# Kernel optimization log

Measured on AMD Instinct MI355X. Metric: run time of the kernel, lower is better.

Reference implementation:

```python
import jax, jax.numpy as jnp
import numpy as np

NU, NI, E = 100000, 100000, 500000  # users, items, edges per edge type
DIN, DH, DOUT = 128, 256, 128


def setup_inputs() -> dict:
    key = jax.random.key(0)
    ks = jax.random.split(key, 18)
    f = lambda k, s: jax.random.normal(k, s, dtype=jnp.float32) * 0.02
    inp = {
        # node embedding tables (x_dict defaults to embedding weights)
        'emb_user': f(ks[0], (NU, DIN)),
        'emb_item': f(ks[1], (NI, DIN)),
        # conv1 params: relation user->item (dst=item) and item->user (dst=user)
        'W1_self_ui': f(ks[2], (DIN, DH)), 'W1_neigh_ui': f(ks[3], (DIN, DH)), 'b1_ui': jnp.zeros((DH,), jnp.float32),
        'W1_self_iu': f(ks[4], (DIN, DH)), 'W1_neigh_iu': f(ks[5], (DIN, DH)), 'b1_iu': jnp.zeros((DH,), jnp.float32),
        # conv2 params
        'W2_self_ui': f(ks[6], (DH, DOUT)), 'W2_neigh_ui': f(ks[7], (DH, DOUT)), 'b2_ui': jnp.zeros((DOUT,), jnp.float32),
        'W2_self_iu': f(ks[8], (DH, DOUT)), 'W2_neigh_iu': f(ks[9], (DH, DOUT)), 'b2_iu': jnp.zeros((DOUT,), jnp.float32),
        # edge lists: e1 = user->item edges, e2 = item->user edges
        'e1_src': jax.random.randint(ks[10], (E,), 0, NU),
        'e1_dst': jax.random.randint(ks[11], (E,), 0, NI),
        'e2_src': jax.random.randint(ks[12], (E,), 0, NI),
        'e2_dst': jax.random.randint(ks[13], (E,), 0, NU),
    }
    return inp


def _sage(h_src, h_dst, e_src, e_dst, W_self, W_neigh, b, n_dst):
    # DGL SAGEConv('mean'): fc_self(h_dst) + fc_neigh(mean_neighbors(h_src)) + bias
    msg = h_src[e_src]                                   # [E, d] gather
    ssum = jax.ops.segment_sum(msg, e_dst, num_segments=n_dst)          # [n_dst, d]
    deg = jax.ops.segment_sum(jnp.ones((e_src.shape[0], 1), h_src.dtype), e_dst, num_segments=n_dst)
    mean = ssum / jnp.maximum(deg, 1.0)                  # zero in-degree -> 0
    return h_dst @ W_self + mean @ W_neigh + b


def reference(emb_user, emb_item,
              W1_self_ui, W1_neigh_ui, b1_ui, W1_self_iu, W1_neigh_iu, b1_iu,
              W2_self_ui, W2_neigh_ui, b2_ui, W2_self_iu, W2_neigh_iu, b2_iu,
              e1_src, e1_dst, e2_src, e2_dst):
    # layer 1 (HeteroGraphConv: each ntype receives from exactly one relation)
    h1_item = jax.nn.leaky_relu(_sage(emb_user, emb_item, e1_src, e1_dst, W1_self_ui, W1_neigh_ui, b1_ui, NI))
    h1_user = jax.nn.leaky_relu(_sage(emb_item, emb_user, e2_src, e2_dst, W1_self_iu, W1_neigh_iu, b1_iu, NU))
    # layer 2
    h2_item = _sage(h1_user, h1_item, e1_src, e1_dst, W2_self_ui, W2_neigh_ui, b2_ui, NI)
    h2_user = _sage(h1_item, h1_user, e2_src, e2_dst, W2_self_iu, W2_neigh_iu, b2_iu, NU)
    return (h2_user, h2_item)
```

## Files before the change

kernel.cpp:

```cpp
#include <hip/hip_runtime.h>
#include <stdint.h>

typedef unsigned short u16;
typedef unsigned int   u32;
typedef __attribute__((ext_vector_type(8))) short bf16x8;
typedef __attribute__((ext_vector_type(4))) float f32x4;
typedef __attribute__((ext_vector_type(8))) unsigned short u16x8;

constexpr int NUc = 100000;
constexpr int NIc = 100000;
constexpr int Ec  = 500000;
constexpr int Mrows = 100000;
constexpr int NB  = (100000 + 255) / 256;

__device__ __forceinline__ u16 f2bf(float f) {
  u32 u = __float_as_uint(f);
  u += 0x7fffu + ((u >> 16) & 1u);
  return (u16)(u >> 16);
}
__device__ __forceinline__ float bf2f(u16 h) { return __uint_as_float(((u32)h) << 16); }

__global__ void prep_all(const float* __restrict__ eu, const float* __restrict__ ei,
                         const float* __restrict__ W1s_ui, const float* __restrict__ W1n_ui,
                         const float* __restrict__ W1s_iu, const float* __restrict__ W1n_iu,
                         const float* __restrict__ W2s_ui, const float* __restrict__ W2n_ui,
                         const float* __restrict__ W2s_iu, const float* __restrict__ W2n_iu,
                         u16* __restrict__ ue, u16* __restrict__ ie,
                         u16* __restrict__ Wt1_ui, u16* __restrict__ Wt1_iu,
                         u16* __restrict__ Wt2c_u, u16* __restrict__ Wt2c_i) {
  constexpr int N4 = NUc * 128 / 4;
  constexpr int TOT = 2 * N4 + 262144;
  int i = blockIdx.x * blockDim.x + threadIdx.x;
  const int stride = gridDim.x * blockDim.x;
  for (int t = i; t < TOT; t += stride) {
    if (t < 2 * N4) {
      const float* src = (t < N4) ? eu : ei;
      u16* dst = (t < N4) ? ue : ie;
      int c = (t < N4) ? t : t - N4;
      float4 v = reinterpret_cast<const float4*>(src)[c];
      ushort4 o;
      o.x = f2bf(v.x); o.y = f2bf(v.y); o.z = f2bf(v.z); o.w = f2bf(v.w);
      reinterpret_cast<ushort4*>(dst)[c] = o;
    } else {
      int j = t - 2 * N4;
      if (j < 131072) {
        const float* Ws = (j < 65536) ? W1s_ui : W1s_iu;
        const float* Wn = (j < 65536) ? W1n_ui : W1n_iu;
        u16* dst = (j < 65536) ? Wt1_ui : Wt1_iu;
        int q = j & 65535;
        int n = q >> 8, k = q & 255;
        dst[q] = f2bf(k < 128 ? Ws[k * 256 + n] : Wn[(k - 128) * 256 + n]);
      } else {
        int q = j - 131072;
        int which = q >> 16;
        int s = q & 65535;
        int c = s >> 8, k = s & 255;
        float v;
        if (which == 0) v = (c < 128) ? W2n_ui[k * 128 + c] : W2s_iu[k * 128 + (c - 128)];
        else            v = (c < 128) ? W2n_iu[k * 128 + c] : W2s_ui[k * 128 + (c - 128)];
        u16* dst = which ? Wt2c_i : Wt2c_u;
        dst[s] = f2bf(v);
      }
    }
  }
}

__global__ void hist_kernel(const int* __restrict__ e1_dst, const int* __restrict__ e2_dst,
                            int* __restrict__ ideg1, int* __restrict__ ideg2,
                            int* __restrict__ rank1, int* __restrict__ rank2) {
  int i = blockIdx.x * blockDim.x + threadIdx.x;
  const int stride = gridDim.x * blockDim.x;
  for (; i < 2 * Ec; i += stride) {
    if (i < Ec) rank1[i] = atomicAdd(&ideg1[e1_dst[i]], 1);
    else        rank2[i - Ec] = atomicAdd(&ideg2[e2_dst[i - Ec]], 1);
  }
}

__global__ void block_reduce2(const int* __restrict__ ideg1, const int* __restrict__ ideg2,
                              int* __restrict__ bsum1, int* __restrict__ bsum2, int n) {
  const int* deg = blockIdx.y ? ideg2 : ideg1;
  int* bsum = blockIdx.y ? bsum2 : bsum1;
  __shared__ int s[256];
  int t = threadIdx.x, i = blockIdx.x * 256 + t;
  s[t] = (i < n) ? deg[i] : 0;
  __syncthreads();
  for (int st = 128; st > 0; st >>= 1) { if (t < st) s[t] += s[t + st]; __syncthreads(); }
  if (t == 0) bsum[blockIdx.x] = s[0];
}

__global__ void scan_bsums2(const int* __restrict__ bsum1, const int* __restrict__ bsum2,
                            int* __restrict__ bscan1, int* __restrict__ bscan2, int nb) {
  const int* bsum = blockIdx.x ? bsum2 : bsum1;
  int* bscan = blockIdx.x ? bscan2 : bscan1;
  __shared__ int s[512];
  int t = threadIdx.x;
  int v0 = (t < nb) ? bsum[t] : 0;
  s[t] = v0;
  __syncthreads();
  for (int d = 1; d < 512; d <<= 1) {
    int v = (t >= d) ? s[t - d] : 0;
    __syncthreads();
    s[t] += v;
    __syncthreads();
  }
  if (t < nb) bscan[t] = s[t] - v0;
}

__global__ void scan_blocks2(const int* __restrict__ ideg1, const int* __restrict__ ideg2,
                             const int* __restrict__ bscan1, const int* __restrict__ bscan2,
                             int* __restrict__ off1, int* __restrict__ off2, int n) {
  const int* deg = blockIdx.y ? ideg2 : ideg1;
  const int* bscan = blockIdx.y ? bscan2 : bscan1;
  int* off = blockIdx.y ? off2 : off1;
  __shared__ int s[256];
  int t = threadIdx.x, i = blockIdx.x * 256 + t;
  int d = (i < n) ? deg[i] : 0;
  s[t] = d;
  __syncthreads();
  for (int st = 1; st < 256; st <<= 1) {
    int v = (t >= st) ? s[t - st] : 0;
    __syncthreads();
    s[t] += v;
    __syncthreads();
  }
  if (i < n) off[i] = bscan[blockIdx.x] + s[t] - d;
  if (i == 0) off[n] = Ec;
}

__global__ void fill_csr_kernel(const int* __restrict__ e1_src, const int* __restrict__ e1_dst,
                                const int* __restrict__ e2_src, const int* __restrict__ e2_dst,
                                const int* __restrict__ rank1, const int* __restrict__ rank2,
                                const int* __restrict__ off1, const int* __restrict__ off2,
                                int* __restrict__ csr1, int* __restrict__ csr2) {
  int i = blockIdx.x * blockDim.x + threadIdx.x;
  const int stride = gridDim.x * blockDim.x;
  for (; i < 2 * Ec; i += stride) {
    if (i < Ec) {
      int d = e1_dst[i];
      csr1[off1[d] + rank1[i]] = e1_src[i];
    } else {
      int e = i - Ec;
      int d = e2_dst[e];
      csr2[off2[d] + rank2[e]] = e2_src[e];
    }
  }
}

__global__ __launch_bounds__(256) void gather2(const u16* __restrict__ fA, const int* __restrict__ offA,
                                               const int* __restrict__ csrA, u16* __restrict__ outA,
                                               const u16* __restrict__ fB, const int* __restrict__ offB,
                                               const int* __restrict__ csrB, u16* __restrict__ outB) {
  const int wid  = (blockIdx.x * blockDim.x + threadIdx.x) >> 6;
  const int lane = threadIdx.x & 63;
  const u16* f; const int* off; const int* csr; u16* out; int r;
  if (wid < 100000)      { f = fA; off = offA; csr = csrA; out = outA; r = wid; }
  else if (wid < 200000) { f = fB; off = offB; csr = csrB; out = outB; r = wid - 100000; }
  else return;
  const int j0 = off[r], j1 = off[r + 1];
  const int colb = lane << 1;
  float ax = 0.f, ay = 0.f;
  for (int jb = j0; jb < j1; jb += 64) {
    int cnt = min(64, j1 - jb);
    int idx = (jb + lane < j1) ? csr[jb + lane] : 0;
    int t = 0;
    for (; t + 2 <= cnt; t += 2) {
      int s0 = __shfl(idx, t), s1 = __shfl(idx, t + 1);
      u32 v0 = *reinterpret_cast<const u32*>(f + (size_t)s0 * 128 + colb);
      u32 v1 = *reinterpret_cast<const u32*>(f + (size_t)s1 * 128 + colb);
      ax += __uint_as_float(v0 << 16);
      ay += __uint_as_float(v0 & 0xffff0000u);
      ax += __uint_as_float(v1 << 16);
      ay += __uint_as_float(v1 & 0xffff0000u);
    }
    if (t < cnt) {
      int s0 = __shfl(idx, t);
      u32 v0 = *reinterpret_cast<const u32*>(f + (size_t)s0 * 128 + colb);
      ax += __uint_as_float(v0 << 16);
      ay += __uint_as_float(v0 & 0xffff0000u);
    }
  }
  float rs = 1.0f / fmaxf((float)(j1 - j0), 1.0f);
  u32 o = (u32)f2bf(ax * rs) | ((u32)f2bf(ay * rs) << 16);
  *reinterpret_cast<u32*>(out + (size_t)r * 128 + colb) = o;
}

__global__ __launch_bounds__(256) void gather_final(
    const u16* __restrict__ pA, const int* __restrict__ offA, const int* __restrict__ csrA,
    const u16* __restrict__ sA, float* __restrict__ oA,
    const u16* __restrict__ pB, const int* __restrict__ offB, const int* __restrict__ csrB,
    const u16* __restrict__ sB, float* __restrict__ oB) {
  const int wid  = (blockIdx.x * blockDim.x + threadIdx.x) >> 6;
  const int lane = threadIdx.x & 63;
  const u16* f; const int* off; const int* csr; const u16* sf; float* out; int r;
  if (wid < 100000)      { f = pA; off = offA; csr = csrA; sf = sA; out = oA; r = wid; }
  else if (wid < 200000) { f = pB; off = offB; csr = csrB; sf = sB; out = oB; r = wid - 100000; }
  else return;
  const int j0 = off[r], j1 = off[r + 1];
  const int colb = lane << 1;
  float ax = 0.f, ay = 0.f;
  for (int jb = j0; jb < j1; jb += 64) {
    int cnt = min(64, j1 - jb);
    int idx = (jb + lane < j1) ? csr[jb + lane] : 0;
    int t = 0;
    for (; t + 2 <= cnt; t += 2) {
      int s0 = __shfl(idx, t), s1 = __shfl(idx, t + 1);
      u32 v0 = *reinterpret_cast<const u32*>(f + (size_t)s0 * 128 + colb);
      u32 v1 = *reinterpret_cast<const u32*>(f + (size_t)s1 * 128 + colb);
      ax += __uint_as_float(v0 << 16);
      ay += __uint_as_float(v0 & 0xffff0000u);
      ax += __uint_as_float(v1 << 16);
      ay += __uint_as_float(v1 & 0xffff0000u);
    }
    if (t < cnt) {
      int s0 = __shfl(idx, t);
      u32 v0 = *reinterpret_cast<const u32*>(f + (size_t)s0 * 128 + colb);
      ax += __uint_as_float(v0 << 16);
      ay += __uint_as_float(v0 & 0xffff0000u);
    }
  }
  float rs = 1.0f / fmaxf((float)(j1 - j0), 1.0f);
  u32 sv = *reinterpret_cast<const u32*>(sf + (size_t)r * 128 + colb);
  float2 o;
  o.x = ax * rs + __uint_as_float(sv << 16);
  o.y = ay * rs + __uint_as_float(sv & 0xffff0000u);
  *reinterpret_cast<float2*>(out + (size_t)r * 128 + colb) = o;
}

__device__ __forceinline__ void glds16(const void* g, void* l) {
  __builtin_amdgcn_global_load_lds((const __attribute__((address_space(1))) void*)g,
                                   (__attribute__((address_space(3))) void*)l, 16, 0, 0);
}

template<int NTAB, int EPI, int AST>
__global__ __launch_bounds__(256) void mfma_gemm2(
    const u16* __restrict__ A0a, const u16* __restrict__ A1a, const u16* __restrict__ Bta,
    const float* __restrict__ biasa, u16* __restrict__ out0a, u16* __restrict__ out1a,
    const u16* __restrict__ A0b, const u16* __restrict__ A1b, const u16* __restrict__ Btb,
    const float* __restrict__ biasb, u16* __restrict__ out0b, u16* __restrict__ out1b,
    int M)
{
  constexpr int K = 256, BK = 32, BM = 128;
  __shared__ __align__(16) u16 smem[8192];
  u16* As = smem;
  u16* Bs = smem + 4096;

  const bool zb = (blockIdx.z != 0);
  const u16* A0 = zb ? A0b : A0a;
  const u16* A1 = zb ? A1b : A1a;
  const u16* Bt = zb ? Btb : Bta;
  const float* bias = zb ? biasb : biasa;

  const int tid  = threadIdx.x;
  const int lane = tid & 63;
  const int w    = tid >> 6;
  const int wr   = w >> 1, wc = w & 1;
  const int gr0  = blockIdx.x * BM;
  const int gc0  = blockIdx.y * BM;

  f32x4 acc[4][4];
  #pragma unroll
  for (int m = 0; m < 4; ++m)
    #pragma unroll
    for (int n = 0; n < 4; ++n) acc[m][n] = (f32x4){0.f, 0.f, 0.f, 0.f};

  const int srow  = lane >> 2;
  const int sslot = lane & 3;

  for (int kt = 0; kt < K; kt += BK) {
    const u16* At = (NTAB == 2 && kt >= 128) ? A1 : A0;
    const int kbase = (NTAB == 2) ? (kt & 127) : kt;
    #pragma unroll
    for (int c = 0; c < 2; ++c) {
      int rl = w * 32 + c * 16 + srow;
      int swz = (sslot ^ ((rl >> 1) & 3)) << 3;
      int grow = gr0 + rl; grow = grow < M ? grow : M - 1;
      glds16(At + (size_t)grow * AST + kbase + swz, As + (size_t)(w * 32 + c * 16) * BK);
      glds16(Bt + (size_t)(gc0 + rl) * K + kt + swz, Bs + (size_t)(w * 32 + c * 16) * BK);
    }
    __syncthreads();

    bf16x8 af[4], bfr[4];
    #pragma unroll
    for (int m = 0; m < 4; ++m) {
      int row = wr * 64 + m * 16 + (lane & 15);
      int idx = (row << 5) + ((((lane >> 4) ^ ((row >> 1) & 3))) << 3);
      af[m] = *reinterpret_cast<const bf16x8*>(As + idx);
    }
    #pragma unroll
    for (int n = 0; n < 4; ++n) {
      int row = wc * 64 + n * 16 + (lane & 15);
      int idx = (row << 5) + ((((lane >> 4) ^ ((row >> 1) & 3))) << 3);
      bfr[n] = *reinterpret_cast<const bf16x8*>(Bs + idx);
    }
    #pragma unroll
    for (int m = 0; m < 4; ++m)
      #pragma unroll
      for (int n = 0; n < 4; ++n)
        acc[m][n] = __builtin_amdgcn_mfma_f32_16x16x32_bf16(af[m], bfr[n], acc[m][n], 0, 0, 0);
    __syncthreads();
  }

  u16* outp;
  if (EPI == 0) outp = zb ? out0b : out0a;
  else          outp = (blockIdx.y == 0) ? (zb ? out0b : out0a) : (zb ? out1b : out1a);
  const bool useBias = (EPI == 0) || (blockIdx.y == 1);

  const int cLane = lane & 15;
  const int rGrp  = (lane >> 4) << 2;
  for (int s = 0; s < 2; ++s) {
    if (wr == s) {
      #pragma unroll
      for (int n = 0; n < 4; ++n) {
        int lc = wc * 64 + n * 16 + cLane;
        float b = 0.f;
        if (useBias) b = (EPI == 0) ? bias[gc0 + lc] : bias[lc];
        #pragma unroll
        for (int m = 0; m < 4; ++m) {
          int lr = m * 16 + rGrp;
          #pragma unroll
          for (int r = 0; r < 4; ++r) {
            float v = acc[m][n][r] + b;
            if (EPI == 0) v = (v >= 0.f) ? v : 0.01f * v;
            smem[(lr + r) * 128 + lc] = f2bf(v);
          }
        }
      }
    }
    __syncthreads();
    #pragma unroll
    for (int pass = 0; pass < 4; ++pass) {
      int chunk = pass * 256 + tid;
      int row = chunk >> 4, c8 = chunk & 15;
      int G = gr0 + s * 64 + row;
      if (G < M) {
        u16x8 v = *reinterpret_cast<const u16x8*>(smem + row * 128 + c8 * 8);
        if (EPI == 0)
          *reinterpret_cast<u16x8*>(outp + (size_t)G * 256 + gc0 + c8 * 8) = v;
        else
          *reinterpret_cast<u16x8*>(outp + (size_t)G * 128 + c8 * 8) = v;
      }
    }
    if (s == 0) __syncthreads();
  }
}

extern "C" void kernel_launch(void* const* d_in, const int* in_sizes, int n_in,
                              void* d_out, int out_size, void* d_ws, size_t ws_size,
                              hipStream_t stream) {
  const float* emb_user    = (const float*)d_in[0];
  const float* emb_item    = (const float*)d_in[1];
  const float* W1_self_ui  = (const float*)d_in[2];
  const float* W1_neigh_ui = (const float*)d_in[3];
  const float* b1_ui       = (const float*)d_in[4];
  const float* W1_self_iu  = (const float*)d_in[5];
  const float* W1_neigh_iu = (const float*)d_in[6];
  const float* b1_iu       = (const float*)d_in[7];
  const float* W2_self_ui  = (const float*)d_in[8];
  const float* W2_neigh_ui = (const float*)d_in[9];
  const float* b2_ui       = (const float*)d_in[10];
  const float* W2_self_iu  = (const float*)d_in[11];
  const float* W2_neigh_iu = (const float*)d_in[12];
  const float* b2_iu       = (const float*)d_in[13];
  const int* e1_src = (const int*)d_in[14];
  const int* e1_dst = (const int*)d_in[15];
  const int* e2_src = (const int*)d_in[16];
  const int* e2_dst = (const int*)d_in[17];

  u16* p16 = (u16*)d_ws;
  u16* ue     = p16; p16 += (size_t)NUc * 128;
  u16* ie     = p16; p16 += (size_t)NIc * 128;
  u16* h1i    = p16; p16 += (size_t)NIc * 256;
  u16* h1u    = p16; p16 += (size_t)NUc * 256;
  u16* aggb_i = p16; p16 += (size_t)NIc * 128;
  u16* aggb_u = p16; p16 += (size_t)NUc * 128;
  u16* proj_i2u = p16; p16 += (size_t)NIc * 128;
  u16* self_i   = p16; p16 += (size_t)NIc * 128;
  u16* Wt1_ui  = p16; p16 += 256 * 256;
  u16* Wt1_iu  = p16; p16 += 256 * 256;
  u16* Wt2c_u  = p16; p16 += 256 * 256;
  u16* Wt2c_i  = p16; p16 += 256 * 256;
  u16* proj_u2i = aggb_i;
  u16* self_u   = aggb_u;
  int* ip    = (int*)p16;
  int* ideg1 = ip;  ip += NIc;
  int* ideg2 = ip;  ip += NUc;
  int* off1  = ip;  ip += NIc + 1;
  int* off2  = ip;  ip += NUc + 1;
  int* rank1 = ip;  ip += Ec;
  int* rank2 = ip;  ip += Ec;
  int* csr1  = ip;  ip += Ec;
  int* csr2  = ip;  ip += Ec;
  int* bsum1 = ip;  ip += 512;
  int* bscan1= ip;  ip += 512;
  int* bsum2 = ip;  ip += 512;
  int* bscan2= ip;  ip += 512;

  float* h2_user = (float*)d_out;
  float* h2_item = h2_user + (size_t)NUc * 128;

  dim3 blk(256);
  const int gather2Blocks = (200000 + 3) / 4;
  dim3 gemmGrid(782, 2, 2);

  hipMemsetAsync(ideg1, 0, sizeof(int) * (size_t)(NIc + NUc), stream);
  prep_all<<<4096, blk, 0, stream>>>(emb_user, emb_item,
                                     W1_self_ui, W1_neigh_ui, W1_self_iu, W1_neigh_iu,
                                     W2_self_ui, W2_neigh_ui, W2_self_iu, W2_neigh_iu,
                                     ue, ie, Wt1_ui, Wt1_iu, Wt2c_u, Wt2c_i);
  hist_kernel<<<1024, blk, 0, stream>>>(e1_dst, e2_dst, ideg1, ideg2, rank1, rank2);
  block_reduce2<<<dim3(NB, 2), blk, 0, stream>>>(ideg1, ideg2, bsum1, bsum2, NIc);
  scan_bsums2<<<2, 512, 0, stream>>>(bsum1, bsum2, bscan1, bscan2, NB);
  scan_blocks2<<<dim3(NB, 2), blk, 0, stream>>>(ideg1, ideg2, bscan1, bscan2, off1, off2, NIc);
  fill_csr_kernel<<<1024, blk, 0, stream>>>(e1_src, e1_dst, e2_src, e2_dst,
                                            rank1, rank2, off1, off2, csr1, csr2);

  gather2<<<gather2Blocks, blk, 0, stream>>>(ue, off1, csr1, aggb_i,
                                             ie, off2, csr2, aggb_u);
  mfma_gemm2<2, 0, 128><<<gemmGrid, blk, 0, stream>>>(
      ie, aggb_i, Wt1_ui, b1_ui, h1i, nullptr,
      ue, aggb_u, Wt1_iu, b1_iu, h1u, nullptr, Mrows);

  mfma_gemm2<1, 1, 256><<<gemmGrid, blk, 0, stream>>>(
      h1u, nullptr, Wt2c_u, b2_iu, proj_u2i, self_u,
      h1i, nullptr, Wt2c_i, b2_ui, proj_i2u, self_i, Mrows);

  gather_final<<<gather2Blocks, blk, 0, stream>>>(
      proj_u2i, off1, csr1, self_i, h2_item,
      proj_i2u, off2, csr2, self_u, h2_user);
}
```

Baseline: 390.3 us.

## Fuse prep and histogram kernels, unroll gathers by four, add nontemporal memory ops

Merges the bf16 conversion/weight-transpose kernel and the degree histogram kernel into one launch, with block ranges partitioned so the two run concurrently. Unrolls the CSR gather loops in both gather kernels to four outstanding row loads per iteration to raise memory-level parallelism. Adds nontemporal loads and stores for streaming data (embedding reads, edge arrays in CSR fill, final outputs, self-projection GEMM outputs) to reduce cache pollution. The nontemporal hints may hurt if the data is reused soon after, such as the self projections read back by gather_final.

```diff
diff --git a/kernel.cpp b/kernel.cpp
--- a/kernel.cpp
+++ b/kernel.cpp
@@ -5,6 +5,7 @@
 typedef unsigned int   u32;
 typedef __attribute__((ext_vector_type(8))) short bf16x8;
 typedef __attribute__((ext_vector_type(4))) float f32x4;
+typedef __attribute__((ext_vector_type(2))) float f32x2;
 typedef __attribute__((ext_vector_type(8))) unsigned short u16x8;
 
 constexpr int NUc = 100000;
@@ -20,59 +21,62 @@
 }
 __device__ __forceinline__ float bf2f(u16 h) { return __uint_as_float(((u32)h) << 16); }
 
-__global__ void prep_all(const float* __restrict__ eu, const float* __restrict__ ei,
-                         const float* __restrict__ W1s_ui, const float* __restrict__ W1n_ui,
-                         const float* __restrict__ W1s_iu, const float* __restrict__ W1n_iu,
-                         const float* __restrict__ W2s_ui, const float* __restrict__ W2n_ui,
-                         const float* __restrict__ W2s_iu, const float* __restrict__ W2n_iu,
-                         u16* __restrict__ ue, u16* __restrict__ ie,
-                         u16* __restrict__ Wt1_ui, u16* __restrict__ Wt1_iu,
-                         u16* __restrict__ Wt2c_u, u16* __restrict__ Wt2c_i) {
-  constexpr int N4 = NUc * 128 / 4;
-  constexpr int TOT = 2 * N4 + 262144;
-  int i = blockIdx.x * blockDim.x + threadIdx.x;
-  const int stride = gridDim.x * blockDim.x;
-  for (int t = i; t < TOT; t += stride) {
-    if (t < 2 * N4) {
-      const float* src = (t < N4) ? eu : ei;
-      u16* dst = (t < N4) ? ue : ie;
-      int c = (t < N4) ? t : t - N4;
-      float4 v = reinterpret_cast<const float4*>(src)[c];
-      ushort4 o;
-      o.x = f2bf(v.x); o.y = f2bf(v.y); o.z = f2bf(v.z); o.w = f2bf(v.w);
-      reinterpret_cast<ushort4*>(dst)[c] = o;
-    } else {
-      int j = t - 2 * N4;
-      if (j < 131072) {
-        const float* Ws = (j < 65536) ? W1s_ui : W1s_iu;
-        const float* Wn = (j < 65536) ? W1n_ui : W1n_iu;
-        u16* dst = (j < 65536) ? Wt1_ui : Wt1_iu;
-        int q = j & 65535;
-        int n = q >> 8, k = q & 255;
-        dst[q] = f2bf(k < 128 ? Ws[k * 256 + n] : Wn[(k - 128) * 256 + n]);
+constexpr int PREP_B = 4096;
+constexpr int HIST_B = 1024;
+__global__ void prep_hist(const float* __restrict__ eu, const float* __restrict__ ei,
+                          const float* __restrict__ W1s_ui, const float* __restrict__ W1n_ui,
+                          const float* __restrict__ W1s_iu, const float* __restrict__ W1n_iu,
+                          const float* __restrict__ W2s_ui, const float* __restrict__ W2n_ui,
+                          const float* __restrict__ W2s_iu, const float* __restrict__ W2n_iu,
+                          u16* __restrict__ ue, u16* __restrict__ ie,
+                          u16* __restrict__ Wt1_ui, u16* __restrict__ Wt1_iu,
+                          u16* __restrict__ Wt2c_u, u16* __restrict__ Wt2c_i,
+                          const int* __restrict__ e1_dst, const int* __restrict__ e2_dst,
+                          int* __restrict__ ideg1, int* __restrict__ ideg2,
+                          int* __restrict__ rank1, int* __restrict__ rank2) {
+  if (blockIdx.x < PREP_B) {
+    constexpr int N4 = NUc * 128 / 4;
+    constexpr int TOT = 2 * N4 + 262144;
+    int i = blockIdx.x * blockDim.x + threadIdx.x;
+    const int stride = PREP_B * 256;
+    for (int t = i; t < TOT; t += stride) {
+      if (t < 2 * N4) {
+        const float* src = (t < N4) ? eu : ei;
+        u16* dst = (t < N4) ? ue : ie;
+        int c = (t < N4) ? t : t - N4;
+        f32x4 v = __builtin_nontemporal_load(reinterpret_cast<const f32x4*>(src) + c);
+        ushort4 o;
+        o.x = f2bf(v.x); o.y = f2bf(v.y); o.z = f2bf(v.z); o.w = f2bf(v.w);
+        reinterpret_cast<ushort4*>(dst)[c] = o;
       } else {
-        int q = j - 131072;
-        int which = q >> 16;
-        int s = q & 65535;
-        int c = s >> 8, k = s & 255;
-        float v;
-        if (which == 0) v = (c < 128) ? W2n_ui[k * 128 + c] : W2s_iu[k * 128 + (c - 128)];
-        else            v = (c < 128) ? W2n_iu[k * 128 + c] : W2s_ui[k * 128 + (c - 128)];
-        u16* dst = which ? Wt2c_i : Wt2c_u;
-        dst[s] = f2bf(v);
+        int j = t - 2 * N4;
+        if (j < 131072) {
+          const float* Ws = (j < 65536) ? W1s_ui : W1s_iu;
+          const float* Wn = (j < 65536) ? W1n_ui : W1n_iu;
+          u16* dst = (j < 65536) ? Wt1_ui : Wt1_iu;
+          int q = j & 65535;
+          int n = q >> 8, k = q & 255;
+          dst[q] = f2bf(k < 128 ? Ws[k * 256 + n] : Wn[(k - 128) * 256 + n]);
+        } else {
+          int q = j - 131072;
+          int which = q >> 16;
+          int s = q & 65535;
+          int c = s >> 8, k = s & 255;
+          float v;
+          if (which == 0) v = (c < 128) ? W2n_ui[k * 128 + c] : W2s_iu[k * 128 + (c - 128)];
+          else            v = (c < 128) ? W2n_iu[k * 128 + c] : W2s_ui[k * 128 + (c - 128)];
+          u16* dst = which ? Wt2c_i : Wt2c_u;
+          dst[s] = f2bf(v);
+        }
       }
     }
-  }
-}
-
-__global__ void hist_kernel(const int* __restrict__ e1_dst, const int* __restrict__ e2_dst,
-                            int* __restrict__ ideg1, int* __restrict__ ideg2,
-                            int* __restrict__ rank1, int* __restrict__ rank2) {
-  int i = blockIdx.x * blockDim.x + threadIdx.x;
-  const int stride = gridDim.x * blockDim.x;
-  for (; i < 2 * Ec; i += stride) {
-    if (i < Ec) rank1[i] = atomicAdd(&ideg1[e1_dst[i]], 1);
-    else        rank2[i - Ec] = atomicAdd(&ideg2[e2_dst[i - Ec]], 1);
+  } else {
+    int i = (blockIdx.x - PREP_B) * blockDim.x + threadIdx.x;
+    const int stride = HIST_B * 256;
+    for (; i < 2 * Ec; i += stride) {
+      if (i < Ec) rank1[i] = atomicAdd(&ideg1[e1_dst[i]], 1);
+      else        rank2[i - Ec] = atomicAdd(&ideg2[e2_dst[i - Ec]], 1);
+    }
   }
 }
 
@@ -136,12 +140,14 @@
   const int stride = gridDim.x * blockDim.x;
   for (; i < 2 * Ec; i += stride) {
     if (i < Ec) {
-      int d = e1_dst[i];
-      csr1[off1[d] + rank1[i]] = e1_src[i];
+      int d = __builtin_nontemporal_load(e1_dst + i);
+      int r = __builtin_nontemporal_load(rank1 + i);
+      csr1[off1[d] + r] = __builtin_nontemporal_load(e1_src + i);
     } else {
       int e = i - Ec;
-      int d = e2_dst[e];
-      csr2[off2[d] + rank2[e]] = e2_src[e];
+      int d = __builtin_nontemporal_load(e2_dst + e);
+      int r = __builtin_nontemporal_load(rank2 + e);
+      csr2[off2[d] + r] = __builtin_nontemporal_load(e2_src + e);
     }
   }
 }
@@ -163,16 +169,19 @@
     int cnt = min(64, j1 - jb);
     int idx = (jb + lane < j1) ? csr[jb + lane] : 0;
     int t = 0;
-    for (; t + 2 <= cnt; t += 2) {
-      int s0 = __shfl(idx, t), s1 = __shfl(idx, t + 1);
+    for (; t + 4 <= cnt; t += 4) {
+      int s0 = __shfl(idx, t),     s1 = __shfl(idx, t + 1);
+      int s2 = __shfl(idx, t + 2), s3 = __shfl(idx, t + 3);
       u32 v0 = *reinterpret_cast<const u32*>(f + (size_t)s0 * 128 + colb);
       u32 v1 = *reinterpret_cast<const u32*>(f + (size_t)s1 * 128 + colb);
-      ax += __uint_as_float(v0 << 16);
-      ay += __uint_as_float(v0 & 0xffff0000u);
-      ax += __uint_as_float(v1 << 16);
-      ay += __uint_as_float(v1 & 0xffff0000u);
-    }
-    if (t < cnt) {
+      u32 v2 = *reinterpret_cast<const u32*>(f + (size_t)s2 * 128 + colb);
+      u32 v3 = *reinterpret_cast<const u32*>(f + (size_t)s3 * 128 + colb);
+      ax += __uint_as_float(v0 << 16) + __uint_as_float(v1 << 16)
+          + __uint_as_float(v2 << 16) + __uint_as_float(v3 << 16);
+      ay += __uint_as_float(v0 & 0xffff0000u) + __uint_as_float(v1 & 0xffff0000u)
+          + __uint_as_float(v2 & 0xffff0000u) + __uint_as_float(v3 & 0xffff0000u);
+    }
+    for (; t < cnt; ++t) {
       int s0 = __shfl(idx, t);
       u32 v0 = *reinterpret_cast<const u32*>(f + (size_t)s0 * 128 + colb);
       ax += __uint_as_float(v0 << 16);
@@ -202,16 +211,19 @@
     int cnt = min(64, j1 - jb);
     int idx = (jb + lane < j1) ? csr[jb + lane] : 0;
     int t = 0;
-    for (; t + 2 <= cnt; t += 2) {
-      int s0 = __shfl(idx, t), s1 = __shfl(idx, t + 1);
+    for (; t + 4 <= cnt; t += 4) {
+      int s0 = __shfl(idx, t),     s1 = __shfl(idx, t + 1);
+      int s2 = __shfl(idx, t + 2), s3 = __shfl(idx, t + 3);
       u32 v0 = *reinterpret_cast<const u32*>(f + (size_t)s0 * 128 + colb);
       u32 v1 = *reinterpret_cast<const u32*>(f + (size_t)s1 * 128 + colb);
-      ax += __uint_as_float(v0 << 16);
-      ay += __uint_as_float(v0 & 0xffff0000u);
-      ax += __uint_as_float(v1 << 16);
-      ay += __uint_as_float(v1 & 0xffff0000u);
-    }
-    if (t < cnt) {
+      u32 v2 = *reinterpret_cast<const u32*>(f + (size_t)s2 * 128 + colb);
+      u32 v3 = *reinterpret_cast<const u32*>(f + (size_t)s3 * 128 + colb);
+      ax += __uint_as_float(v0 << 16) + __uint_as_float(v1 << 16)
+          + __uint_as_float(v2 << 16) + __uint_as_float(v3 << 16);
+      ay += __uint_as_float(v0 & 0xffff0000u) + __uint_as_float(v1 & 0xffff0000u)
+          + __uint_as_float(v2 & 0xffff0000u) + __uint_as_float(v3 & 0xffff0000u);
+    }
+    for (; t < cnt; ++t) {
       int s0 = __shfl(idx, t);
       u32 v0 = *reinterpret_cast<const u32*>(f + (size_t)s0 * 128 + colb);
       ax += __uint_as_float(v0 << 16);
@@ -219,11 +231,11 @@
     }
   }
   float rs = 1.0f / fmaxf((float)(j1 - j0), 1.0f);
-  u32 sv = *reinterpret_cast<const u32*>(sf + (size_t)r * 128 + colb);
-  float2 o;
+  u32 sv = __builtin_nontemporal_load(reinterpret_cast<const u32*>(sf + (size_t)r * 128 + colb));
+  f32x2 o;
   o.x = ax * rs + __uint_as_float(sv << 16);
   o.y = ay * rs + __uint_as_float(sv & 0xffff0000u);
-  *reinterpret_cast<float2*>(out + (size_t)r * 128 + colb) = o;
+  __builtin_nontemporal_store(o, reinterpret_cast<f32x2*>(out + (size_t)r * 128 + colb));
 }
 
 __device__ __forceinline__ void glds16(const void* g, void* l) {
@@ -304,6 +316,7 @@
   if (EPI == 0) outp = zb ? out0b : out0a;
   else          outp = (blockIdx.y == 0) ? (zb ? out0b : out0a) : (zb ? out1b : out1a);
   const bool useBias = (EPI == 0) || (blockIdx.y == 1);
+  const bool ntStore = (EPI == 1) && (blockIdx.y == 1);
 
   const int cLane = lane & 15;
   const int rGrp  = (lane >> 4) << 2;
@@ -336,6 +349,8 @@
         u16x8 v = *reinterpret_cast<const u16x8*>(smem + row * 128 + c8 * 8);
         if (EPI == 0)
           *reinterpret_cast<u16x8*>(outp + (size_t)G * 256 + gc0 + c8 * 8) = v;
+        else if (ntStore)
+          __builtin_nontemporal_store(v, reinterpret_cast<u16x8*>(outp + (size_t)G * 128 + c8 * 8));
         else
           *reinterpret_cast<u16x8*>(outp + (size_t)G * 128 + c8 * 8) = v;
       }
@@ -403,11 +418,12 @@
   dim3 gemmGrid(782, 2, 2);
 
   hipMemsetAsync(ideg1, 0, sizeof(int) * (size_t)(NIc + NUc), stream);
-  prep_all<<<4096, blk, 0, stream>>>(emb_user, emb_item,
-                                     W1_self_ui, W1_neigh_ui, W1_self_iu, W1_neigh_iu,
-                                     W2_self_ui, W2_neigh_ui, W2_self_iu, W2_neigh_iu,
-                                     ue, ie, Wt1_ui, Wt1_iu, Wt2c_u, Wt2c_i);
-  hist_kernel<<<1024, blk, 0, stream>>>(e1_dst, e2_dst, ideg1, ideg2, rank1, rank2);
+  prep_hist<<<PREP_B + HIST_B, blk, 0, stream>>>(
+      emb_user, emb_item,
+      W1_self_ui, W1_neigh_ui, W1_self_iu, W1_neigh_iu,
+      W2_self_ui, W2_neigh_ui, W2_self_iu, W2_neigh_iu,
+      ue, ie, Wt1_ui, Wt1_iu, Wt2c_u, Wt2c_i,
+      e1_dst, e2_dst, ideg1, ideg2, rank1, rank2);
   block_reduce2<<<dim3(NB, 2), blk, 0, stream>>>(ideg1, ideg2, bsum1, bsum2, NIc);
   scan_bsums2<<<2, 512, 0, stream>>>(bsum1, bsum2, bscan1, bscan2, NB);
   scan_blocks2<<<dim3(NB, 2), blk, 0, stream>>>(ideg1, ideg2, bscan1, bscan2, off1, off2, NIc);
```

Result: faster. 365.4 us (-6.4%).
